# Kernel tuning notes

Hardware: AMD Instinct MI355X
Metric: run time of the kernel (lower is better)

Reference implementation:

```python
import jax, jax.numpy as jnp
import numpy as np
from jax import lax

B, T, D, U, SIG = 256, 1024, 256, 128, 20

def setup_inputs() -> dict:
    key = jax.random.key(0)
    ks = jax.random.split(key, 6)
    return {
        "inputs": jax.random.normal(ks[0], (B, T, D), dtype=jnp.float32),
        "signatures": jax.random.normal(ks[1], (B, T, SIG), dtype=jnp.float32),
        "input_kernel": jax.random.normal(ks[2], (D, 3 * U), dtype=jnp.float32) * 0.05,
        "recurrent_kernel": jax.random.normal(ks[3], (U, 3 * U), dtype=jnp.float32) * 0.05,
        "forget_kernel": jax.random.normal(ks[4], (SIG, U), dtype=jnp.float32) * 0.05,
        "bias": jnp.zeros((4 * U,), dtype=jnp.float32),
    }

def reference(inputs, signatures, input_kernel, recurrent_kernel, forget_kernel, bias):
    # inputs: [B,T,D], signatures: [B,T,SIG]
    b, t, d = inputs.shape
    u = recurrent_kernel.shape[0]
    b_i, b_f, b_c, b_o = jnp.split(bias, 4, axis=-1)
    h0 = jnp.zeros((b, u), dtype=inputs.dtype)
    c0 = jnp.zeros((b, u), dtype=inputs.dtype)
    # precompute the time-parallel projections (same math as per-step)
    x_proj = jnp.einsum('btd,du->btu', inputs, input_kernel)            # [B,T,3U]
    f_seq = jax.nn.sigmoid(jnp.einsum('bts,su->btu', signatures, forget_kernel) + b_f)  # [B,T,U]

    def step(carry, xs):
        x_t, f_t = xs                     # [B,3U], [B,U]
        h_prev, c_prev = carry
        gates = jnp.dot(h_prev, recurrent_kernel) + x_t
        i_t, c_hat, o_t = jnp.split(gates, 3, axis=-1)
        i_t = jax.nn.sigmoid(i_t + b_i)
        c_hat = jnp.tanh(c_hat + b_c)
        o_t = jax.nn.sigmoid(o_t + b_o)
        c_new = f_t * c_prev + i_t * c_hat
        h_new = o_t * jnp.tanh(c_new)
        return (h_new, c_new), h_new

    scan_xs = (x_proj.transpose(1, 0, 2), f_seq.transpose(1, 0, 2))    # time-major
    (_, _), h_seq = lax.scan(step, (h0, c0), scan_xs)
    return h_seq.transpose(1, 0, 2)                                    # [B,T,U]
```

## Files before the change

### kernel.cpp

```cpp
#include <hip/hip_runtime.h>

typedef _Float16 f16;
typedef _Float16 f16x2 __attribute__((ext_vector_type(2)));
typedef _Float16 f16x8 __attribute__((ext_vector_type(8)));
typedef float f32x4 __attribute__((ext_vector_type(4)));

#define NB 256
#define NT 1024
#define ND 256
#define NU 128
#define NSIG 20
#define N3U 384
#define BT (NB * NT)
#define CH 16
#define NCHUNK (NT / CH)

static __device__ __forceinline__ float sigmoid_fast(float x) {
    return __builtin_amdgcn_rcpf(1.f + __expf(-x));
}
static __device__ __forceinline__ float tanh_fast(float x) {
    return 1.f - 2.f * __builtin_amdgcn_rcpf(__expf(2.f * x) + 1.f);
}

__global__ __launch_bounds__(256) void xproj_gemm(
    const float* __restrict__ A,
    const float* __restrict__ Wk,
    f16* __restrict__ out)
{
    const int n0 = blockIdx.x * 64;
    const int m0 = blockIdx.y * 64;
    const int tid = threadIdx.x;
    const int lane = tid & 63;
    const int w = tid >> 6;
    const int mm = lane & 15;
    const int q = lane >> 4;

    __shared__ __align__(16) f16 sA[64 * 40];
    __shared__ __align__(16) f16 sB[64 * 40];

    f32x4 acc[4] = {{0.f,0.f,0.f,0.f},{0.f,0.f,0.f,0.f},{0.f,0.f,0.f,0.f},{0.f,0.f,0.f,0.f}};

    const int ar = tid >> 2;
    const int ac = (tid & 3) * 8;
    const int bn = tid & 63;
    const int bkc = (tid >> 6) * 8;

    for (int kt = 0; kt < ND; kt += 32) {
        const float4 a0 = *(const float4*)(A + (size_t)(m0 + ar) * ND + kt + ac);
        const float4 a1 = *(const float4*)(A + (size_t)(m0 + ar) * ND + kt + ac + 4);
        f16x8 av;
        av[0]=(f16)a0.x; av[1]=(f16)a0.y; av[2]=(f16)a0.z; av[3]=(f16)a0.w;
        av[4]=(f16)a1.x; av[5]=(f16)a1.y; av[6]=(f16)a1.z; av[7]=(f16)a1.w;
        *(f16x8*)(sA + ar * 40 + ac) = av;

        f16x8 bv;
        #pragma unroll
        for (int i = 0; i < 8; ++i)
            bv[i] = (f16)Wk[(size_t)(kt + bkc + i) * N3U + n0 + bn];
        *(f16x8*)(sB + bn * 40 + bkc) = bv;

        __syncthreads();

        f16x8 afrag = *(const f16x8*)(sA + (w * 16 + mm) * 40 + q * 8);
        #pragma unroll
        for (int nt = 0; nt < 4; ++nt) {
            f16x8 bfrag = *(const f16x8*)(sB + (nt * 16 + mm) * 40 + q * 8);
            acc[nt] = __builtin_amdgcn_mfma_f32_16x16x32_f16(afrag, bfrag, acc[nt], 0, 0, 0);
        }
        __syncthreads();
    }

    #pragma unroll
    for (int nt = 0; nt < 4; ++nt) {
        #pragma unroll
        for (int r = 0; r < 4; ++r) {
            const int row = m0 + w * 16 + q * 4 + r;
            const int col = n0 + nt * 16 + mm;
            out[(size_t)row * N3U + col] = (f16)acc[nt][r];
        }
    }
}

__global__ __launch_bounds__(256) void fgate_kernel(
    const float* __restrict__ sig,
    const float* __restrict__ Wf,
    const float* __restrict__ bias,
    f16* __restrict__ fout)
{
    const int gid = blockIdx.x * 256 + threadIdx.x;
    const int u = gid & 127;
    const int bt = gid >> 7;
    float acc = bias[NU + u];
    #pragma unroll
    for (int s = 0; s < NSIG; ++s)
        acc += sig[(size_t)bt * NSIG + s] * Wf[s * NU + u];
    fout[gid] = (f16)sigmoid_fast(acc);
}

__global__ __launch_bounds__(384, 2) void recur_kernel(
    const f16* __restrict__ xp,
    const f16* __restrict__ fg,
    const float* __restrict__ Wr,
    const float* __restrict__ bias,
    float* __restrict__ out)
{
    const int b = blockIdx.x;
    const int j = threadIdx.x;

    __shared__ __align__(16) f16 x_sh[2][CH * N3U];
    __shared__ __align__(16) f16 f_sh[2][CH * NU];
    __shared__ __align__(16) float o_sh[CH * NU];
    __shared__ __align__(16) f16 h_sh[2][NU];
    __shared__ __align__(16) float gate_sh[N3U];

    f16x2 wr[64];
    #pragma unroll
    for (int k2 = 0; k2 < 64; ++k2) {
        const float w0 = Wr[(size_t)(2 * k2) * N3U + j];
        const float w1 = Wr[(size_t)(2 * k2 + 1) * N3U + j];
        f16x2 p; p[0] = (f16)w0; p[1] = (f16)w1;
        wr[k2] = p;
    }

    float bi = 0.f, bc = 0.f, bo = 0.f, cstate = 0.f;
    if (j < NU) {
        bi = bias[j];
        bc = bias[2 * NU + j];
        bo = bias[3 * NU + j];
        h_sh[0][j] = (f16)0.f;
    }

    {
        const uint4* xsrc = (const uint4*)(xp + ((size_t)b * NT) * N3U);
        uint4* xdst = (uint4*)x_sh[0];
        xdst[j] = xsrc[j];
        xdst[j + 384] = xsrc[j + 384];
        if (j < 256) {
            const uint4* fsrc = (const uint4*)(fg + ((size_t)b * NT) * NU);
            ((uint4*)f_sh[0])[j] = fsrc[j];
        }
    }
    __syncthreads();

    int p = 0;
    for (int c = 0; c < NCHUNK; ++c) {
        const int bb = c & 1;

        uint4 xs0, xs1, fs0;
        const bool have_next = (c + 1 < NCHUNK);
        if (have_next) {
            const uint4* xsrc = (const uint4*)(xp + ((size_t)b * NT + (size_t)(c + 1) * CH) * N3U);
            xs0 = xsrc[j];
            xs1 = xsrc[j + 384];
            if (j < 256) {
                const uint4* fsrc = (const uint4*)(fg + ((size_t)b * NT + (size_t)(c + 1) * CH) * NU);
                fs0 = fsrc[j];
            }
        }

        for (int t = 0; t < CH; ++t) {
            float g0 = (float)x_sh[bb][t * N3U + j], g1 = 0.f, g2 = 0.f, g3 = 0.f;
            const uint4* h4 = (const uint4*)h_sh[p];
            #pragma unroll
            for (int kk = 0; kk < 16; ++kk) {
                const uint4 hv = h4[kk];
                g0 = __builtin_amdgcn_fdot2(__builtin_bit_cast(f16x2, hv.x), wr[kk * 4 + 0], g0, false);
                g1 = __builtin_amdgcn_fdot2(__builtin_bit_cast(f16x2, hv.y), wr[kk * 4 + 1], g1, false);
                g2 = __builtin_amdgcn_fdot2(__builtin_bit_cast(f16x2, hv.z), wr[kk * 4 + 2], g2, false);
                g3 = __builtin_amdgcn_fdot2(__builtin_bit_cast(f16x2, hv.w), wr[kk * 4 + 3], g3, false);
            }
            gate_sh[j] = (g0 + g1) + (g2 + g3);
            __syncthreads();

            if (j < NU) {
                const float gi = gate_sh[j] + bi;
                const float gc = gate_sh[j + NU] + bc;
                const float go = gate_sh[j + 2 * NU] + bo;
                const float it = sigmoid_fast(gi);
                const float chv = tanh_fast(gc);
                const float ot = sigmoid_fast(go);
                const float ft = (float)f_sh[bb][t * NU + j];
                cstate = ft * cstate + it * chv;
                const float h = ot * tanh_fast(cstate);
                o_sh[t * NU + j] = h;
                h_sh[p ^ 1][j] = (f16)h;
            }
            __syncthreads();
            p ^= 1;
        }

        {
            uint4* dst = (uint4*)(out + ((size_t)b * NT + (size_t)c * CH) * NU);
            const uint4* src = (const uint4*)o_sh;
            if (j < 256) {
                dst[j] = src[j];
                dst[j + 256] = src[j + 256];
            }
        }

        if (have_next) {
            uint4* xdst = (uint4*)x_sh[bb ^ 1];
            xdst[j] = xs0;
            xdst[j + 384] = xs1;
            if (j < 256) ((uint4*)f_sh[bb ^ 1])[j] = fs0;
        }
        __syncthreads();
    }
}

extern "C" void kernel_launch(void* const* d_in, const int* in_sizes, int n_in,
                              void* d_out, int out_size, void* d_ws, size_t ws_size,
                              hipStream_t stream) {
    const float* inputs = (const float*)d_in[0];
    const float* sig    = (const float*)d_in[1];
    const float* Wk     = (const float*)d_in[2];
    const float* Wr     = (const float*)d_in[3];
    const float* Wf     = (const float*)d_in[4];
    const float* bias   = (const float*)d_in[5];
    float* out = (float*)d_out;

    f16* xp = (f16*)d_ws;
    f16* fg = (f16*)((char*)d_ws + (size_t)BT * N3U * sizeof(f16));

    xproj_gemm<<<dim3(N3U / 64, BT / 64), 256, 0, stream>>>(inputs, Wk, xp);
    fgate_kernel<<<dim3((BT * NU) / 256), 256, 0, stream>>>(sig, Wf, bias, fg);
    recur_kernel<<<dim3(NB), 384, 0, stream>>>(xp, fg, Wr, bias, out);

    (void)in_sizes; (void)n_in; (void)out_size; (void)ws_size;
}
```

Before: 1.339 ms.

## Enlarge projection GEMM tiles and stage forget-gate weights in shared memory

Result: faster. 1.198 ms (-10.6%).

```diff
diff --git a/kernel.cpp b/kernel.cpp
--- a/kernel.cpp
+++ b/kernel.cpp
@@ -2,6 +2,7 @@
 
 typedef _Float16 f16;
 typedef _Float16 f16x2 __attribute__((ext_vector_type(2)));
+typedef _Float16 f16x4 __attribute__((ext_vector_type(4)));
 typedef _Float16 f16x8 __attribute__((ext_vector_type(8)));
 typedef float f32x4 __attribute__((ext_vector_type(4)));
 
@@ -15,6 +16,11 @@
 #define CH 16
 #define NCHUNK (NT / CH)
 
+#define BM 128
+#define BN 128
+#define BK 32
+#define LDK 40
+
 static __device__ __forceinline__ float sigmoid_fast(float x) {
     return __builtin_amdgcn_rcpf(1.f + __expf(-x));
 }
@@ -27,56 +33,87 @@
     const float* __restrict__ Wk,
     f16* __restrict__ out)
 {
-    const int n0 = blockIdx.x * 64;
-    const int m0 = blockIdx.y * 64;
+    const int n0 = blockIdx.x * BN;
+    const int m0 = blockIdx.y * BM;
     const int tid = threadIdx.x;
     const int lane = tid & 63;
     const int w = tid >> 6;
     const int mm = lane & 15;
     const int q = lane >> 4;
-
-    __shared__ __align__(16) f16 sA[64 * 40];
-    __shared__ __align__(16) f16 sB[64 * 40];
-
-    f32x4 acc[4] = {{0.f,0.f,0.f,0.f},{0.f,0.f,0.f,0.f},{0.f,0.f,0.f,0.f},{0.f,0.f,0.f,0.f}};
-
-    const int ar = tid >> 2;
-    const int ac = (tid & 3) * 8;
-    const int bn = tid & 63;
-    const int bkc = (tid >> 6) * 8;
-
-    for (int kt = 0; kt < ND; kt += 32) {
-        const float4 a0 = *(const float4*)(A + (size_t)(m0 + ar) * ND + kt + ac);
-        const float4 a1 = *(const float4*)(A + (size_t)(m0 + ar) * ND + kt + ac + 4);
-        f16x8 av;
-        av[0]=(f16)a0.x; av[1]=(f16)a0.y; av[2]=(f16)a0.z; av[3]=(f16)a0.w;
-        av[4]=(f16)a1.x; av[5]=(f16)a1.y; av[6]=(f16)a1.z; av[7]=(f16)a1.w;
-        *(f16x8*)(sA + ar * 40 + ac) = av;
-
-        f16x8 bv;
+    const int wr = w >> 1;
+    const int wc = w & 1;
+
+    __shared__ __align__(16) f16 sA[BM * LDK];
+    __shared__ __align__(16) f16 sB[BN * LDK];
+
+    f32x4 acc[4][4];
+    #pragma unroll
+    for (int i = 0; i < 4; ++i)
+        #pragma unroll
+        for (int j = 0; j < 4; ++j)
+            acc[i][j] = (f32x4){0.f, 0.f, 0.f, 0.f};
+
+    const int ar = tid >> 1;
+    const int ac = (tid & 1) * 16;
+    const int bn = tid >> 1;
+    const int bk = (tid & 1) * 16;
+
+    for (int kt = 0; kt < ND; kt += BK) {
+        const float* ap = A + (size_t)(m0 + ar) * ND + kt + ac;
+        const float4 a0 = *(const float4*)(ap + 0);
+        const float4 a1 = *(const float4*)(ap + 4);
+        const float4 a2 = *(const float4*)(ap + 8);
+        const float4 a3 = *(const float4*)(ap + 12);
+
+        f16x8 bv0, bv1;
         #pragma unroll
         for (int i = 0; i < 8; ++i)
-            bv[i] = (f16)Wk[(size_t)(kt + bkc + i) * N3U + n0 + bn];
-        *(f16x8*)(sB + bn * 40 + bkc) = bv;
+            bv0[i] = (f16)Wk[(size_t)(kt + bk + i) * N3U + n0 + bn];
+        #pragma unroll
+        for (int i = 0; i < 8; ++i)
+            bv1[i] = (f16)Wk[(size_t)(kt + bk + 8 + i) * N3U + n0 + bn];
+
+        f16x8 av0, av1;
+        av0[0]=(f16)a0.x; av0[1]=(f16)a0.y; av0[2]=(f16)a0.z; av0[3]=(f16)a0.w;
+        av0[4]=(f16)a1.x; av0[5]=(f16)a1.y; av0[6]=(f16)a1.z; av0[7]=(f16)a1.w;
+        av1[0]=(f16)a2.x; av1[1]=(f16)a2.y; av1[2]=(f16)a2.z; av1[3]=(f16)a2.w;
+        av1[4]=(f16)a3.x; av1[5]=(f16)a3.y; av1[6]=(f16)a3.z; av1[7]=(f16)a3.w;
+
+        *(f16x8*)(sA + ar * LDK + ac)     = av0;
+        *(f16x8*)(sA + ar * LDK + ac + 8) = av1;
+        *(f16x8*)(sB + bn * LDK + bk)     = bv0;
+        *(f16x8*)(sB + bn * LDK + bk + 8) = bv1;
 
         __syncthreads();
 
-        f16x8 afrag = *(const f16x8*)(sA + (w * 16 + mm) * 40 + q * 8);
-        #pragma unroll
-        for (int nt = 0; nt < 4; ++nt) {
-            f16x8 bfrag = *(const f16x8*)(sB + (nt * 16 + mm) * 40 + q * 8);
-            acc[nt] = __builtin_amdgcn_mfma_f32_16x16x32_f16(afrag, bfrag, acc[nt], 0, 0, 0);
-        }
+        f16x8 afrag[4], bfrag[4];
+        #pragma unroll
+        for (int mi = 0; mi < 4; ++mi)
+            afrag[mi] = *(const f16x8*)(sA + (wr * 64 + mi * 16 + mm) * LDK + q * 8);
+        #pragma unroll
+        for (int ni = 0; ni < 4; ++ni)
+            bfrag[ni] = *(const f16x8*)(sB + (wc * 64 + ni * 16 + mm) * LDK + q * 8);
+
+        #pragma unroll
+        for (int mi = 0; mi < 4; ++mi)
+            #pragma unroll
+            for (int ni = 0; ni < 4; ++ni)
+                acc[mi][ni] = __builtin_amdgcn_mfma_f32_16x16x32_f16(
+                    afrag[mi], bfrag[ni], acc[mi][ni], 0, 0, 0);
+
         __syncthreads();
     }
 
     #pragma unroll
-    for (int nt = 0; nt < 4; ++nt) {
-        #pragma unroll
-        for (int r = 0; r < 4; ++r) {
-            const int row = m0 + w * 16 + q * 4 + r;
-            const int col = n0 + nt * 16 + mm;
-            out[(size_t)row * N3U + col] = (f16)acc[nt][r];
+    for (int mi = 0; mi < 4; ++mi) {
+        #pragma unroll
+        for (int ni = 0; ni < 4; ++ni) {
+            #pragma unroll
+            for (int r = 0; r < 4; ++r) {
+                const int row = m0 + wr * 64 + mi * 16 + q * 4 + r;
+                const int col = n0 + wc * 64 + ni * 16 + mm;
+                out[(size_t)row * N3U + col] = (f16)acc[mi][ni][r];
+            }
         }
     }
 }
@@ -87,14 +124,36 @@
     const float* __restrict__ bias,
     f16* __restrict__ fout)
 {
-    const int gid = blockIdx.x * 256 + threadIdx.x;
-    const int u = gid & 127;
-    const int bt = gid >> 7;
-    float acc = bias[NU + u];
-    #pragma unroll
-    for (int s = 0; s < NSIG; ++s)
-        acc += sig[(size_t)bt * NSIG + s] * Wf[s * NU + u];
-    fout[gid] = (f16)sigmoid_fast(acc);
+    __shared__ float sWf[NSIG * NU];
+    __shared__ float sSig[8 * NSIG];
+    const int tid = threadIdx.x;
+    const int bt0 = blockIdx.x * 8;
+
+    for (int i = tid; i < NSIG * NU; i += 256)
+        sWf[i] = Wf[i];
+    if (tid < 8 * NSIG)
+        sSig[tid] = sig[(size_t)bt0 * NSIG + tid];
+    __syncthreads();
+
+    const int r = tid >> 5;
+    const int u0 = (tid & 31) * 4;
+
+    float a0 = bias[NU + u0 + 0];
+    float a1 = bias[NU + u0 + 1];
+    float a2 = bias[NU + u0 + 2];
+    float a3 = bias[NU + u0 + 3];
+    #pragma unroll
+    for (int s = 0; s < NSIG; ++s) {
+        const float sv = sSig[r * NSIG + s];
+        const float4 wv = *(const float4*)(&sWf[s * NU + u0]);
+        a0 += sv * wv.x; a1 += sv * wv.y; a2 += sv * wv.z; a3 += sv * wv.w;
+    }
+    f16x4 o;
+    o[0] = (f16)sigmoid_fast(a0);
+    o[1] = (f16)sigmoid_fast(a1);
+    o[2] = (f16)sigmoid_fast(a2);
+    o[3] = (f16)sigmoid_fast(a3);
+    *(f16x4*)(&fout[(size_t)(bt0 + r) * NU + u0]) = o;
 }
 
 __global__ __launch_bounds__(384, 2) void recur_kernel(
@@ -222,8 +281,8 @@
     f16* xp = (f16*)d_ws;
     f16* fg = (f16*)((char*)d_ws + (size_t)BT * N3U * sizeof(f16));
 
-    xproj_gemm<<<dim3(N3U / 64, BT / 64), 256, 0, stream>>>(inputs, Wk, xp);
-    fgate_kernel<<<dim3((BT * NU) / 256), 256, 0, stream>>>(sig, Wf, bias, fg);
+    xproj_gemm<<<dim3(N3U / BN, BT / BM), 256, 0, stream>>>(inputs, Wk, xp);
+    fgate_kernel<<<dim3(BT / 8), 256, 0, stream>>>(sig, Wf, bias, fg);
     recur_kernel<<<dim3(NB), 384, 0, stream>>>(xp, fg, Wr, bias, out);
 
     (void)in_sizes; (void)n_in; (void)out_size; (void)ws_size;
```
